# Kernel optimization log

Measured on AMD Instinct MI355X. Metric: run time of the kernel, lower is better.

## Reference

```python
import jax, jax.numpy as jnp
import numpy as np

H = 8  # number of heads


def setup_inputs() -> dict:
    key = jax.random.key(0)
    ks = jax.random.split(key, 5)
    B, L, D = 4, 2048, 512
    scale = 1.0 / np.sqrt(D)
    return {
        "query": jax.random.normal(ks[0], (B, L, D), dtype=jnp.float32),
        "keys": jax.random.normal(ks[1], (B, L, D), dtype=jnp.float32),
        "Wq": jax.random.normal(ks[2], (D, D), dtype=jnp.float32) * scale,
        "Wk": jax.random.normal(ks[3], (D, D), dtype=jnp.float32) * scale,
        "Wv": jax.random.normal(ks[4], (D, D), dtype=jnp.float32) * scale,
    }


def reference(query, keys, Wq, Wk, Wv):
    B, Lq, D = query.shape
    Lk = keys.shape[1]
    dh = D // H
    # Linear layers (torch nn.Linear: y = x @ W.T), then split heads.
    Q = (query @ Wq.T).reshape(B, Lq, H, dh)
    K = (keys @ Wk.T).reshape(B, Lk, H, dh)
    V = (keys @ Wv.T).reshape(B, Lk, H, dh)
    # NOTE: original scales by sqrt(key_dim) == sqrt(D), not sqrt(head_dim).
    inv_scale = 1.0 / jnp.sqrt(jnp.float32(D))
    scores = jnp.einsum("bqhd,bkhd->bhqk", Q, K) * inv_scale  # [B,H,Lq,Lk]
    attn = jax.nn.softmax(scores, axis=-1)
    # dropout_p = 0 (eval); no dropout applied.
    out = jnp.einsum("bhqk,bkhd->bqhd", attn, V).reshape(B, Lq, D)
    return out + query  # residual
```

## Files before the change

kernel.cpp:

```cpp
#include <hip/hip_runtime.h>

typedef unsigned short u16;
typedef unsigned int   u32;
typedef short  s16x8  __attribute__((ext_vector_type(8)));
typedef float  f32x16 __attribute__((ext_vector_type(16)));
typedef unsigned int u32x2 __attribute__((ext_vector_type(2)));

__device__ __forceinline__ u16 f2bf(float f) {
    union { u32 i; float f; } x; x.f = f;
    return (u16)((x.i + 0x8000u) >> 16);
}
__device__ __forceinline__ u32 cvt_pk_bf16(float a, float b) {
    u32 r;
    asm("v_cvt_pk_bf16_f32 %0, %1, %2" : "=v"(r) : "v"(a), "v"(b));
    return r;
}
__device__ __forceinline__ u32x2 pl32_swap2(u32 vdst, u32 vsrc) {
#if __has_builtin(__builtin_amdgcn_permlane32_swap)
    return __builtin_amdgcn_permlane32_swap(vdst, vsrc, false, false);
#else
    asm("v_permlane32_swap_b32 %0, %1" : "+v"(vdst), "+v"(vsrc));
    u32x2 r; r.x = vdst; r.y = vsrc; return r;
#endif
}

#define PD 512

__global__ __launch_bounds__(256) void proj_mfma(
    const float* __restrict__ query, const float* __restrict__ keys,
    const float* __restrict__ Wq, const float* __restrict__ Wk, const float* __restrict__ Wv,
    u16* __restrict__ Qo, u16* __restrict__ Ko, u16* __restrict__ Vt)
{
    const int z = blockIdx.z;
    const float* __restrict__ X = (z == 0) ? query : keys;
    const float* __restrict__ W = (z == 0) ? Wq : ((z == 1) ? Wk : Wv);
    const int bx = blockIdx.x;
    const int by = blockIdx.y;

    const float* __restrict__ Amat = (z < 2) ? X : W;
    const float* __restrict__ Bmat = (z < 2) ? W : X;
    const int a0 = ((z < 2) ? bx : by) * 128;
    const int b0 = ((z < 2) ? by : bx) * 128;

    __shared__ u16 As[128][40];
    __shared__ u16 Bs[128][40];

    const int tid  = threadIdx.x;
    const int wave = tid >> 6, lane = tid & 63;
    const int wm = wave >> 1, wn = wave & 1;
    const int l31 = lane & 31, lh = lane >> 5;

    const int srow = tid >> 1;
    const int sk   = (tid & 1) * 16;

    f32x16 acc[2][2];
    #pragma unroll
    for (int i = 0; i < 2; ++i)
        #pragma unroll
        for (int j = 0; j < 2; ++j)
            #pragma unroll
            for (int r = 0; r < 16; ++r) acc[i][j][r] = 0.f;

    float4 ra[4], rb[4];
    {
        const float* ap = Amat + (size_t)(a0 + srow) * PD + sk;
        const float* bp = Bmat + (size_t)(b0 + srow) * PD + sk;
        #pragma unroll
        for (int i = 0; i < 4; ++i) {
            ra[i] = *(const float4*)(ap + 4*i);
            rb[i] = *(const float4*)(bp + 4*i);
        }
    }

    for (int k0 = 0; k0 < PD; k0 += 32) {
        __syncthreads();
        {
            u32 aw[8], bw[8];
            #pragma unroll
            for (int i = 0; i < 4; ++i) {
                aw[2*i]   = cvt_pk_bf16(ra[i].x, ra[i].y);
                aw[2*i+1] = cvt_pk_bf16(ra[i].z, ra[i].w);
                bw[2*i]   = cvt_pk_bf16(rb[i].x, rb[i].y);
                bw[2*i+1] = cvt_pk_bf16(rb[i].z, rb[i].w);
            }
            *(uint4*)&As[srow][sk]     = *(uint4*)&aw[0];
            *(uint4*)&As[srow][sk + 8] = *(uint4*)&aw[4];
            *(uint4*)&Bs[srow][sk]     = *(uint4*)&bw[0];
            *(uint4*)&Bs[srow][sk + 8] = *(uint4*)&bw[4];
        }
        if (k0 + 32 < PD) {
            const float* ap = Amat + (size_t)(a0 + srow) * PD + (k0 + 32) + sk;
            const float* bp = Bmat + (size_t)(b0 + srow) * PD + (k0 + 32) + sk;
            #pragma unroll
            for (int i = 0; i < 4; ++i) {
                ra[i] = *(const float4*)(ap + 4*i);
                rb[i] = *(const float4*)(bp + 4*i);
            }
        }
        __syncthreads();

        #pragma unroll
        for (int ks = 0; ks < 2; ++ks) {
            s16x8 af[2], bfr[2];
            #pragma unroll
            for (int mf = 0; mf < 2; ++mf) {
                uint4 v = *(uint4*)&As[wm*64 + mf*32 + l31][ks*16 + lh*8];
                af[mf] = *(s16x8*)&v;
            }
            #pragma unroll
            for (int nf = 0; nf < 2; ++nf) {
                uint4 v = *(uint4*)&Bs[wn*64 + nf*32 + l31][ks*16 + lh*8];
                bfr[nf] = *(s16x8*)&v;
            }
            #pragma unroll
            for (int mf = 0; mf < 2; ++mf)
                #pragma unroll
                for (int nf = 0; nf < 2; ++nf)
                    acc[mf][nf] = __builtin_amdgcn_mfma_f32_32x32x16_bf16(
                        af[mf], bfr[nf], acc[mf][nf], 0, 0, 0);
        }
    }

    const float osc = (z == 0) ? (0.044194173824159216f * 1.4426950408889634f) : 1.0f;
    u16* __restrict__ O = (z == 0) ? Qo : Ko;
    #pragma unroll
    for (int mf = 0; mf < 2; ++mf)
        #pragma unroll
        for (int nf = 0; nf < 2; ++nf)
            #pragma unroll
            for (int r = 0; r < 16; ++r) {
                const int mi = a0 + wm*64 + mf*32 + (r & 3) + 8*(r >> 2) + 4*lh;
                const int ni = b0 + wn*64 + nf*32 + l31;
                const u16 v = f2bf(acc[mf][nf][r] * osc);
                if (z < 2) {
                    O[(size_t)mi * PD + ni] = v;
                } else {
                    const int bb_ = ni >> 11, ll = ni & 2047;
                    Vt[((size_t)(bb_ * 512 + mi)) * 2048 + ll] = v;
                }
            }
}

__global__ __launch_bounds__(256) void attn_mfma(
    const u16* __restrict__ Qp, const u16* __restrict__ Kp, const u16* __restrict__ Vt,
    const float* __restrict__ query, float* __restrict__ out)
{
    const int qt = blockIdx.x;
    const int h  = blockIdx.y;
    const int b  = blockIdx.z;
    const int q0 = qt * 128;
    const int L = 2048;

    __shared__ uint4 lds_u4[36864 / 16];
    u16* Ks   = (u16*)lds_u4;
    u16* Vts  = Ks + 64 * 72;
    float* Oe = (float*)lds_u4;

    const int tid  = threadIdx.x;
    const int wave = tid >> 6, lane = tid & 63;
    const int l31 = lane & 31, lh = lane >> 5;

    const int qrow = b * L + q0 + wave * 32 + l31;
    s16x8 qf[4];
    #pragma unroll
    for (int ds = 0; ds < 4; ++ds) {
        uint4 v = *(const uint4*)(Qp + (size_t)qrow * PD + h*64 + ds*16 + lh*8);
        qf[ds] = *(s16x8*)&v;
    }

    f32x16 ot[2];
    #pragma unroll
    for (int mf = 0; mf < 2; ++mf)
        #pragma unroll
        for (int r = 0; r < 16; ++r) ot[mf][r] = 0.f;
    float l_i = 0.f;

    const int srow = tid >> 2;
    const int sc   = (tid & 3) * 16;

    uint4 rk0, rk1, rv0, rv1;
    {
        const u16* kp = Kp + (size_t)(b*L + srow) * PD + h*64 + sc;
        const u16* vp = Vt + ((size_t)((b*8 + h)*64 + srow)) * 2048 + sc;
        rk0 = *(const uint4*)kp;      rk1 = *(const uint4*)(kp + 8);
        rv0 = *(const uint4*)vp;      rv1 = *(const uint4*)(vp + 8);
    }

    for (int k0 = 0; k0 < L; k0 += 64) {
        __syncthreads();
        *(uint4*)&Ks [srow*72 + sc]     = rk0;
        *(uint4*)&Ks [srow*72 + sc + 8] = rk1;
        *(uint4*)&Vts[srow*72 + sc]     = rv0;
        *(uint4*)&Vts[srow*72 + sc + 8] = rv1;
        if (k0 + 64 < L) {
            const u16* kp = Kp + (size_t)(b*L + (k0+64) + srow) * PD + h*64 + sc;
            const u16* vp = Vt + ((size_t)((b*8 + h)*64 + srow)) * 2048 + (k0+64) + sc;
            rk0 = *(const uint4*)kp;  rk1 = *(const uint4*)(kp + 8);
            rv0 = *(const uint4*)vp;  rv1 = *(const uint4*)(vp + 8);
        }
        __syncthreads();

        f32x16 s[2];
        #pragma unroll
        for (int kf = 0; kf < 2; ++kf) {
            #pragma unroll
            for (int r = 0; r < 16; ++r) s[kf][r] = 0.f;
            #pragma unroll
            for (int ds = 0; ds < 4; ++ds) {
                uint4 av = *(uint4*)&Ks[(kf*32 + l31)*72 + ds*16 + lh*8];
                s[kf] = __builtin_amdgcn_mfma_f32_32x32x16_bf16(
                    *(s16x8*)&av, qf[ds], s[kf], 0, 0, 0);
            }
        }

        float rs = 0.f;
        u32 pq[2][4][2];
        #pragma unroll
        for (int kf = 0; kf < 2; ++kf)
            #pragma unroll
            for (int g = 0; g < 4; ++g) {
                float p0 = __builtin_amdgcn_exp2f(s[kf][4*g+0]);
                float p1 = __builtin_amdgcn_exp2f(s[kf][4*g+1]);
                float p2 = __builtin_amdgcn_exp2f(s[kf][4*g+2]);
                float p3 = __builtin_amdgcn_exp2f(s[kf][4*g+3]);
                rs += (p0 + p1) + (p2 + p3);
                pq[kf][g][0] = cvt_pk_bf16(p0, p1);
                pq[kf][g][1] = cvt_pk_bf16(p2, p3);
            }
        rs += __shfl_xor(rs, 32);
        l_i += rs;

        #pragma unroll
        for (int s4 = 0; s4 < 4; ++s4) {
            const int kf = s4 >> 1, ga = (s4 & 1) * 2;
            u32x2 r0 = pl32_swap2(pq[kf][ga][0], pq[kf][ga+1][0]);
            u32x2 r1 = pl32_swap2(pq[kf][ga][1], pq[kf][ga+1][1]);
            union { u32 w[4]; s16x8 v; } bu;
            bu.w[0] = r0.x; bu.w[1] = r1.x; bu.w[2] = r0.y; bu.w[3] = r1.y;
            #pragma unroll
            for (int mf = 0; mf < 2; ++mf) {
                uint4 av = *(uint4*)&Vts[(mf*32 + l31)*72 + s4*16 + lh*8];
                ot[mf] = __builtin_amdgcn_mfma_f32_32x32x16_bf16(
                    *(s16x8*)&av, bu.v, ot[mf], 0, 0, 0);
            }
        }
    }

    __syncthreads();
    const float inv_l = 1.0f / l_i;
    #pragma unroll
    for (int mf = 0; mf < 2; ++mf)
        #pragma unroll
        for (int g = 0; g < 4; ++g) {
            float4 v;
            v.x = ot[mf][g*4+0] * inv_l;
            v.y = ot[mf][g*4+1] * inv_l;
            v.z = ot[mf][g*4+2] * inv_l;
            v.w = ot[mf][g*4+3] * inv_l;
            const int dh0 = mf*32 + 8*g + 4*lh;
            *(float4*)&Oe[(wave*32 + l31)*68 + dh0] = v;
        }
    __syncthreads();
    {
        const int r  = tid >> 1;
        const int c0 = (tid & 1) * 32;
        const size_t gb = ((size_t)(b*L + q0 + r)) * PD + h*64 + c0;
        #pragma unroll
        for (int i = 0; i < 8; ++i) {
            float4 ov = *(float4*)&Oe[r*68 + c0 + 4*i];
            float4 qv = *(const float4*)(query + gb + 4*i);
            ov.x += qv.x; ov.y += qv.y; ov.z += qv.z; ov.w += qv.w;
            *(float4*)(out + gb + 4*i) = ov;
        }
    }
}

extern "C" void kernel_launch(void* const* d_in, const int* in_sizes, int n_in,
                              void* d_out, int out_size, void* d_ws, size_t ws_size,
                              hipStream_t stream) {
    const float* query = (const float*)d_in[0];
    const float* keys  = (const float*)d_in[1];
    const float* Wq    = (const float*)d_in[2];
    const float* Wk    = (const float*)d_in[3];
    const float* Wv    = (const float*)d_in[4];
    float* out = (float*)d_out;

    u16* Qp = (u16*)d_ws;
    u16* Kp = Qp + (size_t)8192 * 512;
    u16* Vt = Kp + (size_t)8192 * 512;

    proj_mfma<<<dim3(64, 4, 3), 256, 0, stream>>>(query, keys, Wq, Wk, Wv, Qp, Kp, Vt);
    attn_mfma<<<dim3(16, 8, 4), 256, 0, stream>>>(Qp, Kp, Vt, query, out);
}
```

Before: 162.1 us.

## Double-buffer LDS tiles with two-deep register prefetch in projection and attention

Both kernels now keep two LDS buffers and two register staging sets, so the global loads for tile t+2 and the LDS store for tile t+1 are issued while tile t is being computed. This cuts the number of barriers per tile from two to one. MFMA work is wrapped in s_setprio to favour the math waves. The cost is more LDS use in the projection kernel and more VGPRs for the second staging set, which may lower occupancy.

Result: no change. 163.7 us (+1.0%).

```diff
diff --git a/kernel.cpp b/kernel.cpp
--- a/kernel.cpp
+++ b/kernel.cpp
@@ -42,8 +42,8 @@
     const int a0 = ((z < 2) ? bx : by) * 128;
     const int b0 = ((z < 2) ? by : bx) * 128;
 
-    __shared__ u16 As[128][40];
-    __shared__ u16 Bs[128][40];
+    __shared__ u16 As[2][128][40];
+    __shared__ u16 Bs[2][128][40];
 
     const int tid  = threadIdx.x;
     const int wave = tid >> 6, lane = tid & 63;
@@ -61,55 +61,43 @@
             #pragma unroll
             for (int r = 0; r < 16; ++r) acc[i][j][r] = 0.f;
 
-    float4 ra[4], rb[4];
-    {
-        const float* ap = Amat + (size_t)(a0 + srow) * PD + sk;
-        const float* bp = Bmat + (size_t)(b0 + srow) * PD + sk;
-        #pragma unroll
-        for (int i = 0; i < 4; ++i) {
-            ra[i] = *(const float4*)(ap + 4*i);
-            rb[i] = *(const float4*)(bp + 4*i);
-        }
-    }
-
-    for (int k0 = 0; k0 < PD; k0 += 32) {
-        __syncthreads();
-        {
-            u32 aw[8], bw[8];
-            #pragma unroll
-            for (int i = 0; i < 4; ++i) {
-                aw[2*i]   = cvt_pk_bf16(ra[i].x, ra[i].y);
-                aw[2*i+1] = cvt_pk_bf16(ra[i].z, ra[i].w);
-                bw[2*i]   = cvt_pk_bf16(rb[i].x, rb[i].y);
-                bw[2*i+1] = cvt_pk_bf16(rb[i].z, rb[i].w);
-            }
-            *(uint4*)&As[srow][sk]     = *(uint4*)&aw[0];
-            *(uint4*)&As[srow][sk + 8] = *(uint4*)&aw[4];
-            *(uint4*)&Bs[srow][sk]     = *(uint4*)&bw[0];
-            *(uint4*)&Bs[srow][sk + 8] = *(uint4*)&bw[4];
-        }
-        if (k0 + 32 < PD) {
-            const float* ap = Amat + (size_t)(a0 + srow) * PD + (k0 + 32) + sk;
-            const float* bp = Bmat + (size_t)(b0 + srow) * PD + (k0 + 32) + sk;
-            #pragma unroll
-            for (int i = 0; i < 4; ++i) {
-                ra[i] = *(const float4*)(ap + 4*i);
-                rb[i] = *(const float4*)(bp + 4*i);
-            }
-        }
-        __syncthreads();
-
+    const float* apB = Amat + (size_t)(a0 + srow) * PD + sk;
+    const float* bpB = Bmat + (size_t)(b0 + srow) * PD + sk;
+
+    float4 raA[4], rbA[4], raB[4], rbB[4];
+
+#define P_LOADG(k0v, ra, rb) { \
+    const float* ap_ = apB + (k0v); const float* bp_ = bpB + (k0v); \
+    _Pragma("unroll") \
+    for (int i = 0; i < 4; ++i) { \
+        ra[i] = *(const float4*)(ap_ + 4*i); \
+        rb[i] = *(const float4*)(bp_ + 4*i); } }
+
+#define P_STOREL(bi, ra, rb) { \
+    u32 aw[8], bw[8]; \
+    _Pragma("unroll") \
+    for (int i = 0; i < 4; ++i) { \
+        aw[2*i]   = cvt_pk_bf16(ra[i].x, ra[i].y); \
+        aw[2*i+1] = cvt_pk_bf16(ra[i].z, ra[i].w); \
+        bw[2*i]   = cvt_pk_bf16(rb[i].x, rb[i].y); \
+        bw[2*i+1] = cvt_pk_bf16(rb[i].z, rb[i].w); } \
+    *(uint4*)&As[bi][srow][sk]     = *(uint4*)&aw[0]; \
+    *(uint4*)&As[bi][srow][sk + 8] = *(uint4*)&aw[4]; \
+    *(uint4*)&Bs[bi][srow][sk]     = *(uint4*)&bw[0]; \
+    *(uint4*)&Bs[bi][srow][sk + 8] = *(uint4*)&bw[4]; }
+
+    auto compute = [&](int bi) {
         #pragma unroll
         for (int ks = 0; ks < 2; ++ks) {
             s16x8 af[2], bfr[2];
             #pragma unroll
             for (int mf = 0; mf < 2; ++mf) {
-                uint4 v = *(uint4*)&As[wm*64 + mf*32 + l31][ks*16 + lh*8];
+                uint4 v = *(uint4*)&As[bi][wm*64 + mf*32 + l31][ks*16 + lh*8];
                 af[mf] = *(s16x8*)&v;
             }
             #pragma unroll
             for (int nf = 0; nf < 2; ++nf) {
-                uint4 v = *(uint4*)&Bs[wn*64 + nf*32 + l31][ks*16 + lh*8];
+                uint4 v = *(uint4*)&Bs[bi][wn*64 + nf*32 + l31][ks*16 + lh*8];
                 bfr[nf] = *(s16x8*)&v;
             }
             #pragma unroll
@@ -119,6 +107,33 @@
                     acc[mf][nf] = __builtin_amdgcn_mfma_f32_32x32x16_bf16(
                         af[mf], bfr[nf], acc[mf][nf], 0, 0, 0);
         }
+    };
+
+    P_LOADG(0, raA, rbA);
+    P_STOREL(0, raA, rbA);
+    P_LOADG(32, raB, rbB);
+    __syncthreads();
+
+    #pragma unroll 1
+    for (int t = 0; t < 16; t += 2) {
+        {
+            const int kn = (t + 2 < 16) ? (t + 2) * 32 : t * 32;
+            P_LOADG(kn, raA, rbA);
+        }
+        P_STOREL(1, raB, rbB);
+        __builtin_amdgcn_s_setprio(1);
+        compute(0);
+        __builtin_amdgcn_s_setprio(0);
+        __syncthreads();
+        {
+            const int kn = (t + 3 < 16) ? (t + 3) * 32 : (t + 1) * 32;
+            P_LOADG(kn, raB, rbB);
+        }
+        P_STOREL(0, raA, rbA);
+        __builtin_amdgcn_s_setprio(1);
+        compute(1);
+        __builtin_amdgcn_s_setprio(0);
+        __syncthreads();
     }
 
     const float osc = (z == 0) ? (0.044194173824159216f * 1.4426950408889634f) : 1.0f;
@@ -152,8 +167,10 @@
     const int L = 2048;
 
     __shared__ uint4 lds_u4[36864 / 16];
-    u16* Ks   = (u16*)lds_u4;
-    u16* Vts  = Ks + 64 * 72;
+    u16* KsA  = (u16*)lds_u4;
+    u16* VtsA = KsA  + 64 * 72;
+    u16* KsB  = VtsA + 64 * 72;
+    u16* VtsB = KsB  + 64 * 72;
     float* Oe = (float*)lds_u4;
 
     const int tid  = threadIdx.x;
@@ -178,28 +195,24 @@
     const int srow = tid >> 2;
     const int sc   = (tid & 3) * 16;
 
-    uint4 rk0, rk1, rv0, rv1;
-    {
-        const u16* kp = Kp + (size_t)(b*L + srow) * PD + h*64 + sc;
-        const u16* vp = Vt + ((size_t)((b*8 + h)*64 + srow)) * 2048 + sc;
-        rk0 = *(const uint4*)kp;      rk1 = *(const uint4*)(kp + 8);
-        rv0 = *(const uint4*)vp;      rv1 = *(const uint4*)(vp + 8);
-    }
-
-    for (int k0 = 0; k0 < L; k0 += 64) {
-        __syncthreads();
-        *(uint4*)&Ks [srow*72 + sc]     = rk0;
-        *(uint4*)&Ks [srow*72 + sc + 8] = rk1;
-        *(uint4*)&Vts[srow*72 + sc]     = rv0;
-        *(uint4*)&Vts[srow*72 + sc + 8] = rv1;
-        if (k0 + 64 < L) {
-            const u16* kp = Kp + (size_t)(b*L + (k0+64) + srow) * PD + h*64 + sc;
-            const u16* vp = Vt + ((size_t)((b*8 + h)*64 + srow)) * 2048 + (k0+64) + sc;
-            rk0 = *(const uint4*)kp;  rk1 = *(const uint4*)(kp + 8);
-            rv0 = *(const uint4*)vp;  rv1 = *(const uint4*)(vp + 8);
-        }
-        __syncthreads();
-
+    const u16* kpB = Kp + (size_t)(b*L + srow) * PD + h*64 + sc;
+    const u16* vpB = Vt + ((size_t)((b*8 + h)*64 + srow)) * 2048 + sc;
+
+    uint4 rkA0, rkA1, rvA0, rvA1, rkB0, rkB1, rvB0, rvB1;
+
+#define A_LOADG(k0v, rk0, rk1, rv0, rv1) { \
+    const u16* kp_ = kpB + (size_t)(k0v) * PD; \
+    const u16* vp_ = vpB + (k0v); \
+    rk0 = *(const uint4*)kp_;      rk1 = *(const uint4*)(kp_ + 8); \
+    rv0 = *(const uint4*)vp_;      rv1 = *(const uint4*)(vp_ + 8); }
+
+#define A_STOREL(Ks, Vts, rk0, rk1, rv0, rv1) { \
+    *(uint4*)&(Ks)[srow*72 + sc]      = rk0; \
+    *(uint4*)&(Ks)[srow*72 + sc + 8]  = rk1; \
+    *(uint4*)&(Vts)[srow*72 + sc]     = rv0; \
+    *(uint4*)&(Vts)[srow*72 + sc + 8] = rv1; }
+
+    auto compute = [&](const u16* Ks, const u16* Vts) {
         f32x16 s[2];
         #pragma unroll
         for (int kf = 0; kf < 2; ++kf) {
@@ -212,7 +225,6 @@
                     *(s16x8*)&av, qf[ds], s[kf], 0, 0, 0);
             }
         }
-
         float rs = 0.f;
         u32 pq[2][4][2];
         #pragma unroll
@@ -229,7 +241,6 @@
             }
         rs += __shfl_xor(rs, 32);
         l_i += rs;
-
         #pragma unroll
         for (int s4 = 0; s4 < 4; ++s4) {
             const int kf = s4 >> 1, ga = (s4 & 1) * 2;
@@ -244,9 +255,35 @@
                     *(s16x8*)&av, bu.v, ot[mf], 0, 0, 0);
             }
         }
+    };
+
+    A_LOADG(0, rkA0, rkA1, rvA0, rvA1);
+    A_STOREL(KsA, VtsA, rkA0, rkA1, rvA0, rvA1);
+    A_LOADG(64, rkB0, rkB1, rvB0, rvB1);
+    __syncthreads();
+
+    #pragma unroll 1
+    for (int t = 0; t < 32; t += 2) {
+        {
+            const int kn = (t + 2 < 32) ? (t + 2) * 64 : t * 64;
+            A_LOADG(kn, rkA0, rkA1, rvA0, rvA1);
+        }
+        A_STOREL(KsB, VtsB, rkB0, rkB1, rvB0, rvB1);
+        __builtin_amdgcn_s_setprio(1);
+        compute(KsA, VtsA);
+        __builtin_amdgcn_s_setprio(0);
+        __syncthreads();
+        {
+            const int kn = (t + 3 < 32) ? (t + 3) * 64 : (t + 1) * 64;
+            A_LOADG(kn, rkB0, rkB1, rvB0, rvB1);
+        }
+        A_STOREL(KsA, VtsA, rkA0, rkA1, rvA0, rvA1);
+        __builtin_amdgcn_s_setprio(1);
+        compute(KsB, VtsB);
+        __builtin_amdgcn_s_setprio(0);
+        __syncthreads();
     }
 
-    __syncthreads();
     const float inv_l = 1.0f / l_i;
     #pragma unroll
     for (int mf = 0; mf < 2; ++mf)
```

## Split attention KV loop across two wave groups with double-buffered LDS

Applied to the files above, without the earlier changes.

The attention kernel now launches 512 threads per block as two groups of four waves. Each group handles alternate 64-key tiles of the same 128 query rows, and the two partial outputs and row sums are combined through LDS at the end. Each group also double-buffers its K/V tiles in LDS, with s_setprio raised around the MFMA compute. The aim is more waves per query tile and better overlap of global loads with MFMA work, at the price of twice the LDS per block (lower occupancy) and an extra reduction step.

Result: slower. 166.6 us (+2.8%).

```diff
diff --git a/kernel.cpp b/kernel.cpp
--- a/kernel.cpp
+++ b/kernel.cpp
@@ -141,7 +141,7 @@
             }
 }
 
-__global__ __launch_bounds__(256) void attn_mfma(
+__global__ __launch_bounds__(512) void attn_mfma(
     const u16* __restrict__ Qp, const u16* __restrict__ Kp, const u16* __restrict__ Vt,
     const float* __restrict__ query, float* __restrict__ out)
 {
@@ -151,16 +151,23 @@
     const int q0 = qt * 128;
     const int L = 2048;
 
-    __shared__ uint4 lds_u4[36864 / 16];
-    u16* Ks   = (u16*)lds_u4;
-    u16* Vts  = Ks + 64 * 72;
-    float* Oe = (float*)lds_u4;
+    __shared__ uint4 lds_u4[73728 / 16];
+    u16* lds16 = (u16*)lds_u4;
 
     const int tid  = threadIdx.x;
-    const int wave = tid >> 6, lane = tid & 63;
+    const int wave = tid >> 6;
+    const int grp  = wave >> 2;
+    const int sw   = wave & 3;
+    const int lane = tid & 63;
     const int l31 = lane & 31, lh = lane >> 5;
 
-    const int qrow = b * L + q0 + wave * 32 + l31;
+    u16* gb16 = lds16 + grp * 18432;
+    u16* KsA  = gb16;
+    u16* VtsA = gb16 + 4608;
+    u16* KsB  = gb16 + 9216;
+    u16* VtsB = gb16 + 13824;
+
+    const int qrow = b * L + q0 + sw * 32 + l31;
     s16x8 qf[4];
     #pragma unroll
     for (int ds = 0; ds < 4; ++ds) {
@@ -175,31 +182,28 @@
         for (int r = 0; r < 16; ++r) ot[mf][r] = 0.f;
     float l_i = 0.f;
 
-    const int srow = tid >> 2;
-    const int sc   = (tid & 3) * 16;
-
-    uint4 rk0, rk1, rv0, rv1;
-    {
-        const u16* kp = Kp + (size_t)(b*L + srow) * PD + h*64 + sc;
-        const u16* vp = Vt + ((size_t)((b*8 + h)*64 + srow)) * 2048 + sc;
-        rk0 = *(const uint4*)kp;      rk1 = *(const uint4*)(kp + 8);
-        rv0 = *(const uint4*)vp;      rv1 = *(const uint4*)(vp + 8);
-    }
-
-    for (int k0 = 0; k0 < L; k0 += 64) {
-        __syncthreads();
-        *(uint4*)&Ks [srow*72 + sc]     = rk0;
-        *(uint4*)&Ks [srow*72 + sc + 8] = rk1;
-        *(uint4*)&Vts[srow*72 + sc]     = rv0;
-        *(uint4*)&Vts[srow*72 + sc + 8] = rv1;
-        if (k0 + 64 < L) {
-            const u16* kp = Kp + (size_t)(b*L + (k0+64) + srow) * PD + h*64 + sc;
-            const u16* vp = Vt + ((size_t)((b*8 + h)*64 + srow)) * 2048 + (k0+64) + sc;
-            rk0 = *(const uint4*)kp;  rk1 = *(const uint4*)(kp + 8);
-            rv0 = *(const uint4*)vp;  rv1 = *(const uint4*)(vp + 8);
-        }
-        __syncthreads();
-
+    const int gtid = tid & 255;
+    const int srow = gtid >> 2;
+    const int sc   = (gtid & 3) * 16;
+
+    const u16* kpB = Kp + (size_t)(b*L + grp*64 + srow) * PD + h*64 + sc;
+    const u16* vpB = Vt + ((size_t)((b*8 + h)*64 + srow)) * 2048 + grp*64 + sc;
+
+    uint4 rkA0, rkA1, rvA0, rvA1, rkB0, rkB1, rvB0, rvB1;
+
+#define A_LOADG(k0v, rk0, rk1, rv0, rv1) { \
+    const u16* kp_ = kpB + (size_t)(k0v) * PD; \
+    const u16* vp_ = vpB + (k0v); \
+    rk0 = *(const uint4*)kp_;      rk1 = *(const uint4*)(kp_ + 8); \
+    rv0 = *(const uint4*)vp_;      rv1 = *(const uint4*)(vp_ + 8); }
+
+#define A_STOREL(Ks, Vts, rk0, rk1, rv0, rv1) { \
+    *(uint4*)&(Ks)[srow*72 + sc]      = rk0; \
+    *(uint4*)&(Ks)[srow*72 + sc + 8]  = rk1; \
+    *(uint4*)&(Vts)[srow*72 + sc]     = rv0; \
+    *(uint4*)&(Vts)[srow*72 + sc + 8] = rv1; }
+
+    auto compute = [&](const u16* Ks, const u16* Vts) {
         f32x16 s[2];
         #pragma unroll
         for (int kf = 0; kf < 2; ++kf) {
@@ -212,7 +216,6 @@
                     *(s16x8*)&av, qf[ds], s[kf], 0, 0, 0);
             }
         }
-
         float rs = 0.f;
         u32 pq[2][4][2];
         #pragma unroll
@@ -229,7 +232,6 @@
             }
         rs += __shfl_xor(rs, 32);
         l_i += rs;
-
         #pragma unroll
         for (int s4 = 0; s4 < 4; ++s4) {
             const int kf = s4 >> 1, ga = (s4 & 1) * 2;
@@ -244,29 +246,76 @@
                     *(s16x8*)&av, bu.v, ot[mf], 0, 0, 0);
             }
         }
-    }
-
+    };
+
+    A_LOADG(0, rkA0, rkA1, rvA0, rvA1);
+    A_STOREL(KsA, VtsA, rkA0, rkA1, rvA0, rvA1);
+    A_LOADG(128, rkB0, rkB1, rvB0, rvB1);
     __syncthreads();
-    const float inv_l = 1.0f / l_i;
-    #pragma unroll
-    for (int mf = 0; mf < 2; ++mf)
-        #pragma unroll
-        for (int g = 0; g < 4; ++g) {
-            float4 v;
-            v.x = ot[mf][g*4+0] * inv_l;
-            v.y = ot[mf][g*4+1] * inv_l;
-            v.z = ot[mf][g*4+2] * inv_l;
-            v.w = ot[mf][g*4+3] * inv_l;
-            const int dh0 = mf*32 + 8*g + 4*lh;
-            *(float4*)&Oe[(wave*32 + l31)*68 + dh0] = v;
-        }
+
+    #pragma unroll 1
+    for (int j = 0; j < 16; j += 2) {
+        {
+            const int kn = (j + 2 < 16) ? (j + 2) * 128 : j * 128;
+            A_LOADG(kn, rkA0, rkA1, rvA0, rvA1);
+        }
+        A_STOREL(KsB, VtsB, rkB0, rkB1, rvB0, rvB1);
+        __builtin_amdgcn_s_setprio(1);
+        compute(KsA, VtsA);
+        __builtin_amdgcn_s_setprio(0);
+        __syncthreads();
+        {
+            const int kn = (j + 3 < 16) ? (j + 3) * 128 : (j + 1) * 128;
+            A_LOADG(kn, rkB0, rkB1, rvB0, rvB1);
+        }
+        A_STOREL(KsA, VtsA, rkA0, rkA1, rvA0, rvA1);
+        __builtin_amdgcn_s_setprio(1);
+        compute(KsB, VtsB);
+        __builtin_amdgcn_s_setprio(0);
+        __syncthreads();
+    }
+
+    float* Ppart = (float*)lds_u4;
+    float* l_p   = Ppart + 128*68;
+    float* Oe    = (float*)lds_u4 + 36864/4;
+
+    if (grp == 1) {
+        #pragma unroll
+        for (int mf = 0; mf < 2; ++mf)
+            #pragma unroll
+            for (int g = 0; g < 4; ++g) {
+                float4 v;
+                v.x = ot[mf][g*4+0]; v.y = ot[mf][g*4+1];
+                v.z = ot[mf][g*4+2]; v.w = ot[mf][g*4+3];
+                const int dh0 = mf*32 + 8*g + 4*lh;
+                *(float4*)&Ppart[(sw*32 + l31)*68 + dh0] = v;
+            }
+        if (lh == 0) l_p[sw*32 + l31] = l_i;
+    }
+    __syncthreads();
+    if (grp == 0) {
+        const float inv_l = 1.0f / (l_i + l_p[sw*32 + l31]);
+        #pragma unroll
+        for (int mf = 0; mf < 2; ++mf)
+            #pragma unroll
+            for (int g = 0; g < 4; ++g) {
+                const int dh0 = mf*32 + 8*g + 4*lh;
+                float4 pv = *(float4*)&Ppart[(sw*32 + l31)*68 + dh0];
+                float4 v;
+                v.x = (ot[mf][g*4+0] + pv.x) * inv_l;
+                v.y = (ot[mf][g*4+1] + pv.y) * inv_l;
+                v.z = (ot[mf][g*4+2] + pv.z) * inv_l;
+                v.w = (ot[mf][g*4+3] + pv.w) * inv_l;
+                *(float4*)&Oe[(sw*32 + l31)*68 + dh0] = v;
+            }
+    }
     __syncthreads();
     {
-        const int r  = tid >> 1;
-        const int c0 = (tid & 1) * 32;
+        const int r  = tid >> 2;
+        const int c0 = (tid & 3) * 16;
         const size_t gb = ((size_t)(b*L + q0 + r)) * PD + h*64 + c0;
         #pragma unroll
-        for (int i = 0; i < 8; ++i) {
+        for (int i = 0; i < 4; ++i) {
             float4 ov = *(float4*)&Oe[r*68 + c0 + 4*i];
             float4 qv = *(const float4*)(query + gb + 4*i);
             ov.x += qv.x; ov.y += qv.y; ov.z += qv.z; ov.w += qv.w;
@@ -290,5 +339,5 @@
     u16* Vt = Kp + (size_t)8192 * 512;
 
     proj_mfma<<<dim3(64, 4, 3), 256, 0, stream>>>(query, keys, Wq, Wk, Wv, Qp, Kp, Vt);
-    attn_mfma<<<dim3(16, 8, 4), 256, 0, stream>>>(Qp, Kp, Vt, query, out);
-}
+    attn_mfma<<<dim3(16, 8, 4), 512, 0, stream>>>(Qp, Kp, Vt, query, out);
+}
```
